# Kernel optimization log

Hardware: AMD Instinct MI355X
Metric: run time of the kernel (lower is better)

The kernel has to match this reference:

```python
import jax, jax.numpy as jnp
import numpy as np

N, D, H = 32768, 512, 8
HD = D // H  # head_dim = 64
LN_EPS = 1e-5


def setup_inputs() -> dict:
    key = jax.random.key(0)
    ks = jax.random.split(key, 5)
    s = 1.0 / np.sqrt(D)
    return {
        "h": jax.random.normal(ks[0], (N, D), dtype=jnp.float32),
        "Wq": jax.random.normal(ks[1], (D, D), dtype=jnp.float32) * s,
        "Wk": jax.random.normal(ks[2], (D, D), dtype=jnp.float32) * s,
        "Wv": jax.random.normal(ks[3], (D, D), dtype=jnp.float32) * s,
        "Wf": jax.random.normal(ks[4], (D, D), dtype=jnp.float32) * s,
        "ln_gamma": jnp.ones((D,), dtype=jnp.float32),
        "ln_beta": jnp.zeros((D,), dtype=jnp.float32),
    }


def _layernorm(x, g, b):
    mu = jnp.mean(x, axis=-1, keepdims=True)
    var = jnp.mean(jnp.square(x - mu), axis=-1, keepdims=True)
    return (x - mu) * jax.lax.rsqrt(var + LN_EPS) * g + b


def reference(h, Wq, Wk, Wv, Wf, ln_gamma, ln_beta):
    n = h.shape[0]
    # projections (torch Linear y = x @ W^T; weights here stored as [in,out])
    q = jax.nn.relu((h @ Wq).reshape(n, H, HD))
    k = jax.nn.relu((h @ Wk).reshape(n, H, HD))
    v = (h @ Wv).reshape(n, H, HD)
    # per-node outer-product accumulation over heads (n = head axis here)
    kv = jnp.einsum('bnd,bne->bde', k, v)          # [N, HD, HD]
    num = jnp.einsum('bnd,bde->bne', q, kv)        # [N, H, HD]
    denom = jnp.einsum('bnd,bd->bn', q, k.sum(axis=1))  # [N, H]
    attn = num / denom[..., None]                  # [N, H, HD]
    fh = attn.reshape(n, D) @ Wf                   # dropout = identity (eval)
    out = _layernorm(h + fh, ln_gamma, ln_beta)
    return (out, q, k, v)
```

## Files before the change

kernel.cpp:

```cpp
#include <hip/hip_runtime.h>
#include <hip/hip_bf16.h>

#define NROWS 32768
#define DIM   512
#define HEADS 8
#define LN_EPS 1e-5f

typedef __attribute__((ext_vector_type(8))) short short8;
typedef __attribute__((ext_vector_type(4))) float floatx4;

typedef __attribute__((address_space(3))) void lds_void;
typedef __attribute__((address_space(1))) void gbl_void;

__device__ __forceinline__ void async16(const void* g, void* l) {
    __builtin_amdgcn_global_load_lds(
        (gbl_void*)(unsigned long long)(uintptr_t)g,
        (lds_void*)(unsigned int)(uintptr_t)l,
        16, 0, 0);
}

__global__ __launch_bounds__(256) void hconv_kernel(
    const float* __restrict__ h, __hip_bfloat16* __restrict__ hb)
{
    const size_t i = ((size_t)blockIdx.x * 256 + threadIdx.x) * 4;
    const float4 f = *(const float4*)(h + i);
    union { ushort4 u; __hip_bfloat16 b[4]; } pk;
    pk.b[0] = __float2bfloat16(f.x);
    pk.b[1] = __float2bfloat16(f.y);
    pk.b[2] = __float2bfloat16(f.z);
    pk.b[3] = __float2bfloat16(f.w);
    *(ushort4*)(hb + i) = pk.u;
}

__global__ __launch_bounds__(256) void wtrans_kernel(
    const float* __restrict__ W, __hip_bfloat16* __restrict__ Wt)
{
    __shared__ float tile[32][33];
    const int bn = blockIdx.x * 32;
    const int bk = blockIdx.y * 32;
    const int tx = threadIdx.x & 31;
    const int ty = threadIdx.x >> 5;
    #pragma unroll
    for (int i = ty; i < 32; i += 8)
        tile[i][tx] = W[(size_t)(bk + i) * DIM + bn + tx];
    __syncthreads();
    #pragma unroll
    for (int i = ty; i < 32; i += 8)
        Wt[(size_t)(bn + i) * DIM + bk + tx] = __float2bfloat16(tile[tx][i]);
}

__global__ __launch_bounds__(256) void mfma_gemm_kernel(
    const __hip_bfloat16* __restrict__ A,
    const __hip_bfloat16* __restrict__ Bt,
    float* __restrict__ C, int relu)
{
    __shared__ __align__(16) char smem[16384];

    const int t    = threadIdx.x;
    const int lane = t & 63;
    const int w    = t >> 6;
    const int wm   = w >> 1, wn = w & 1;
    const int l16  = lane & 15, quad = lane >> 4;
    const int bm   = blockIdx.y * 128;
    const int bn   = blockIdx.x * 128;

    const int c0 = w * 128 + lane;
    const int c1 = c0 + 64;
    const int r0 = c0 >> 2, kq0 = (c0 & 3) ^ ((r0 >> 1) & 3);
    const int r1 = c1 >> 2, kq1 = (c1 & 3) ^ ((r1 >> 1) & 3);

    const __hip_bfloat16* gA0 = A  + (size_t)(bm + r0) * DIM + kq0 * 8;
    const __hip_bfloat16* gA1 = A  + (size_t)(bm + r1) * DIM + kq1 * 8;
    const __hip_bfloat16* gB0 = Bt + (size_t)(bn + r0) * DIM + kq0 * 8;
    const __hip_bfloat16* gB1 = Bt + (size_t)(bn + r1) * DIM + kq1 * 8;

    char* dA0 = smem + (w * 128 +  0) * 16;
    char* dA1 = smem + (w * 128 + 64) * 16;
    char* dB0 = smem + 8192 + (w * 128 +  0) * 16;
    char* dB1 = smem + 8192 + (w * 128 + 64) * 16;

    int aoff[4], boff[4];
    #pragma unroll
    for (int i = 0; i < 4; ++i) {
        const int ra = wm * 64 + i * 16 + l16;
        aoff[i] = (ra * 4 + (quad ^ ((ra >> 1) & 3))) * 16;
        const int rb = wn * 64 + i * 16 + l16;
        boff[i] = 8192 + (rb * 4 + (quad ^ ((rb >> 1) & 3))) * 16;
    }

    floatx4 acc[4][4];
    #pragma unroll
    for (int i = 0; i < 4; ++i)
        #pragma unroll
        for (int j = 0; j < 4; ++j)
            acc[i][j] = (floatx4){0.f, 0.f, 0.f, 0.f};

    for (int k0 = 0; k0 < DIM; k0 += 32) {
        async16(gA0 + k0, dA0);
        async16(gA1 + k0, dA1);
        async16(gB0 + k0, dB0);
        async16(gB1 + k0, dB1);
        __syncthreads();

        short8 af[4], bf[4];
        #pragma unroll
        for (int i = 0; i < 4; ++i) af[i] = *(const short8*)(smem + aoff[i]);
        #pragma unroll
        for (int j = 0; j < 4; ++j) bf[j] = *(const short8*)(smem + boff[j]);

        #pragma unroll
        for (int i = 0; i < 4; ++i)
            #pragma unroll
            for (int j = 0; j < 4; ++j)
                acc[i][j] = __builtin_amdgcn_mfma_f32_16x16x32_bf16(
                    af[i], bf[j], acc[i][j], 0, 0, 0);

        __syncthreads();
    }

    #pragma unroll
    for (int i = 0; i < 4; ++i) {
        const int gr = bm + wm * 64 + i * 16 + quad * 4;
        #pragma unroll
        for (int j = 0; j < 4; ++j) {
            const int gc = bn + wn * 64 + j * 16 + l16;
            #pragma unroll
            for (int rg = 0; rg < 4; ++rg) {
                float vv = acc[i][j][rg];
                if (relu) vv = fmaxf(vv, 0.f);
                C[(size_t)(gr + rg) * DIM + gc] = vv;
            }
        }
    }
}

__global__ __launch_bounds__(256) void attn_kernel(
    const float* __restrict__ q, const float* __restrict__ k,
    const float* __restrict__ v, __hip_bfloat16* __restrict__ attn)
{
    __shared__ float sq[2][DIM], sk[2][DIM], sv[2][DIM];
    __shared__ float skv[2][64][68];
    __shared__ float sksum[2][64];

    const int t = threadIdx.x;
    const int r = t >> 7;
    const int u = t & 127;
    const size_t base = ((size_t)blockIdx.x * 2 + r) * DIM;

    ((float4*)sq[r])[u] = ((const float4*)(q + base))[u];
    ((float4*)sk[r])[u] = ((const float4*)(k + base))[u];
    ((float4*)sv[r])[u] = ((const float4*)(v + base))[u];
    __syncthreads();

    const int e0 = (u & 15) * 4;
    const int d0 = (u >> 4) * 8;

    if (u < 64) {
        float s = 0.f;
        #pragma unroll
        for (int h = 0; h < HEADS; ++h) s += sk[r][h * 64 + u];
        sksum[r][u] = s;
    }

    float4 acc[8];
    #pragma unroll
    for (int i = 0; i < 8; ++i) acc[i] = make_float4(0.f, 0.f, 0.f, 0.f);
    #pragma unroll
    for (int h = 0; h < HEADS; ++h) {
        const float4 v4 = *(const float4*)&sv[r][h * 64 + e0];
        #pragma unroll
        for (int i = 0; i < 8; ++i) {
            const float kd = sk[r][h * 64 + d0 + i];
            acc[i].x += kd * v4.x; acc[i].y += kd * v4.y;
            acc[i].z += kd * v4.z; acc[i].w += kd * v4.w;
        }
    }
    #pragma unroll
    for (int i = 0; i < 8; ++i)
        *(float4*)&skv[r][d0 + i][e0] = acc[i];
    __syncthreads();

    const int n = u >> 4;
    float sx = 0.f, sy = 0.f, sz = 0.f, sw = 0.f, den = 0.f;
    #pragma unroll 8
    for (int d = 0; d < 64; ++d) {
        const float qd = sq[r][n * 64 + d];
        const float4 kv4 = *(const float4*)&skv[r][d][e0];
        sx += qd * kv4.x; sy += qd * kv4.y;
        sz += qd * kv4.z; sw += qd * kv4.w;
        den += qd * sksum[r][d];
    }
    union { ushort4 us; __hip_bfloat16 b[4]; } pk;
    pk.b[0] = __float2bfloat16(sx / den);
    pk.b[1] = __float2bfloat16(sy / den);
    pk.b[2] = __float2bfloat16(sz / den);
    pk.b[3] = __float2bfloat16(sw / den);
    *(ushort4*)(attn + base + n * 64 + e0) = pk.us;
}

__global__ __launch_bounds__(256) void ln_kernel(
    const float* __restrict__ h, const float* fh,
    const float* __restrict__ gamma, const float* __restrict__ beta,
    float* out)
{
    const int lane = threadIdx.x & 63;
    const int wave = threadIdx.x >> 6;
    const size_t base = ((size_t)blockIdx.x * 4 + wave) * DIM;

    float x[8];
    float s = 0.f;
    #pragma unroll
    for (int i = 0; i < 8; ++i) {
        const int j = lane + i * 64;
        x[i] = h[base + j] + fh[base + j];
        s += x[i];
    }
    #pragma unroll
    for (int off = 32; off > 0; off >>= 1) s += __shfl_down(s, off);
    const float mu = __shfl(s, 0) * (1.f / DIM);

    float vs = 0.f;
    #pragma unroll
    for (int i = 0; i < 8; ++i) { const float d = x[i] - mu; vs += d * d; }
    #pragma unroll
    for (int off = 32; off > 0; off >>= 1) vs += __shfl_down(vs, off);
    const float rstd = rsqrtf(__shfl(vs, 0) * (1.f / DIM) + LN_EPS);

    #pragma unroll
    for (int i = 0; i < 8; ++i) {
        const int j = lane + i * 64;
        out[base + j] = (x[i] - mu) * rstd * gamma[j] + beta[j];
    }
}

extern "C" void kernel_launch(void* const* d_in, const int* in_sizes, int n_in,
                              void* d_out, int out_size, void* d_ws, size_t ws_size,
                              hipStream_t stream)
{
    const float* h     = (const float*)d_in[0];
    const float* Wq    = (const float*)d_in[1];
    const float* Wk    = (const float*)d_in[2];
    const float* Wv    = (const float*)d_in[3];
    const float* Wf    = (const float*)d_in[4];
    const float* gamma = (const float*)d_in[5];
    const float* beta  = (const float*)d_in[6];

    const size_t ND = (size_t)NROWS * DIM;
    float* out = (float*)d_out;
    float* qo  = out + ND;
    float* ko  = out + 2 * ND;
    float* vo  = out + 3 * ND;
    float* fh  = out;

    __hip_bfloat16* hb  = (__hip_bfloat16*)d_ws;
    __hip_bfloat16* wtq = hb + ND;
    __hip_bfloat16* wtk = wtq + DIM * DIM;
    __hip_bfloat16* wtv = wtk + DIM * DIM;
    __hip_bfloat16* wtf = wtv + DIM * DIM;
    __hip_bfloat16* attnb = hb;

    const dim3 ggrid(DIM / 128, NROWS / 128);
    const dim3 wgrid(16, 16);

    hconv_kernel<<<NROWS * DIM / 1024, 256, 0, stream>>>(h, hb);
    wtrans_kernel<<<wgrid, 256, 0, stream>>>(Wq, wtq);
    wtrans_kernel<<<wgrid, 256, 0, stream>>>(Wk, wtk);
    wtrans_kernel<<<wgrid, 256, 0, stream>>>(Wv, wtv);
    wtrans_kernel<<<wgrid, 256, 0, stream>>>(Wf, wtf);

    mfma_gemm_kernel<<<ggrid, 256, 0, stream>>>(hb, wtq, qo, 1);
    mfma_gemm_kernel<<<ggrid, 256, 0, stream>>>(hb, wtk, ko, 1);
    mfma_gemm_kernel<<<ggrid, 256, 0, stream>>>(hb, wtv, vo, 0);

    attn_kernel<<<NROWS / 2, 256, 0, stream>>>(qo, ko, vo, attnb);

    mfma_gemm_kernel<<<ggrid, 256, 0, stream>>>(attnb, wtf, fh, 0);

    ln_kernel<<<NROWS / 4, 256, 0, stream>>>(h, fh, gamma, beta, out);
}
```

Baseline: 542.6 us.

## Reassociate attention via head scores, fuse QKV GEMM, widen K tile

Rewrites the per-node attention to compute an 8x8 q·k score matrix and weight v by normalized scores, avoiding the 64x64 kv outer-product accumulation. Merges the Q/K/V projections into one GEMM launch writing to three outputs, doubles the GEMM K-step to 64 with a wider LDS swizzle, and combines the four weight transposes into one launch. Layernorm loads/stores are vectorised to float4. Reassociation changes rounding order slightly; doubled LDS use may reduce occupancy.

```diff
diff --git a/kernel.cpp b/kernel.cpp
--- a/kernel.cpp
+++ b/kernel.cpp
@@ -33,9 +33,15 @@
 }
 
 __global__ __launch_bounds__(256) void wtrans_kernel(
-    const float* __restrict__ W, __hip_bfloat16* __restrict__ Wt)
+    const float* __restrict__ Wq, const float* __restrict__ Wk,
+    const float* __restrict__ Wv, const float* __restrict__ Wf,
+    __hip_bfloat16* __restrict__ Wt)
 {
     __shared__ float tile[32][33];
+    const int z = blockIdx.z;
+    const float* W = (z == 0) ? Wq : (z == 1) ? Wk : (z == 2) ? Wv : Wf;
+    __hip_bfloat16* dst = Wt + (size_t)z * DIM * DIM;
+
     const int bn = blockIdx.x * 32;
     const int bk = blockIdx.y * 32;
     const int tx = threadIdx.x & 31;
@@ -46,15 +52,15 @@
     __syncthreads();
     #pragma unroll
     for (int i = ty; i < 32; i += 8)
-        Wt[(size_t)(bn + i) * DIM + bk + tx] = __float2bfloat16(tile[tx][i]);
+        dst[(size_t)(bn + i) * DIM + bk + tx] = __float2bfloat16(tile[tx][i]);
 }
 
 __global__ __launch_bounds__(256) void mfma_gemm_kernel(
     const __hip_bfloat16* __restrict__ A,
     const __hip_bfloat16* __restrict__ Bt,
-    float* __restrict__ C, int relu)
-{
-    __shared__ __align__(16) char smem[16384];
+    float* __restrict__ C, int qkv)
+{
+    __shared__ __align__(16) char smem[32768];
 
     const int t    = threadIdx.x;
     const int lane = t & 63;
@@ -62,31 +68,42 @@
     const int wm   = w >> 1, wn = w & 1;
     const int l16  = lane & 15, quad = lane >> 4;
     const int bm   = blockIdx.y * 128;
-    const int bn   = blockIdx.x * 128;
-
-    const int c0 = w * 128 + lane;
-    const int c1 = c0 + 64;
-    const int r0 = c0 >> 2, kq0 = (c0 & 3) ^ ((r0 >> 1) & 3);
-    const int r1 = c1 >> 2, kq1 = (c1 & 3) ^ ((r1 >> 1) & 3);
-
-    const __hip_bfloat16* gA0 = A  + (size_t)(bm + r0) * DIM + kq0 * 8;
-    const __hip_bfloat16* gA1 = A  + (size_t)(bm + r1) * DIM + kq1 * 8;
-    const __hip_bfloat16* gB0 = Bt + (size_t)(bn + r0) * DIM + kq0 * 8;
-    const __hip_bfloat16* gB1 = Bt + (size_t)(bn + r1) * DIM + kq1 * 8;
-
-    char* dA0 = smem + (w * 128 +  0) * 16;
-    char* dA1 = smem + (w * 128 + 64) * 16;
-    char* dB0 = smem + 8192 + (w * 128 +  0) * 16;
-    char* dB1 = smem + 8192 + (w * 128 + 64) * 16;
-
-    int aoff[4], boff[4];
-    #pragma unroll
-    for (int i = 0; i < 4; ++i) {
-        const int ra = wm * 64 + i * 16 + l16;
-        aoff[i] = (ra * 4 + (quad ^ ((ra >> 1) & 3))) * 16;
-        const int rb = wn * 64 + i * 16 + l16;
-        boff[i] = 8192 + (rb * 4 + (quad ^ ((rb >> 1) & 3))) * 16;
-    }
+    const int bx   = blockIdx.x;
+    const int bn   = bx * 128;
+
+    float* Cp;
+    int ccol, relu;
+    if (qkv) {
+        Cp   = C + (size_t)(bx >> 2) * ((size_t)NROWS * DIM);
+        ccol = (bx & 3) * 128;
+        relu = (bx >> 2) < 2;
+    } else {
+        Cp = C; ccol = bn; relu = 0;
+    }
+
+    int offA[4], offB[4];
+    char* dA[4]; char* dB[4];
+    #pragma unroll
+    for (int s = 0; s < 4; ++s) {
+        const int p = w * 256 + s * 64 + lane;
+        const int r = p >> 3;
+        const int c = (p & 7) ^ (r & 7);
+        offA[s] = (bm + r) * DIM + c * 8;
+        offB[s] = (bn + r) * DIM + c * 8;
+        dA[s] = smem + (w * 256 + s * 64) * 16;
+        dB[s] = smem + 16384 + (w * 256 + s * 64) * 16;
+    }
+
+    int aoff[2][4], boff[2][4];
+    #pragma unroll
+    for (int kk = 0; kk < 2; ++kk)
+        #pragma unroll
+        for (int i = 0; i < 4; ++i) {
+            const int ra = wm * 64 + i * 16 + l16;
+            aoff[kk][i] = (ra * 8 + ((kk * 4 + quad) ^ (ra & 7))) * 16;
+            const int rb = wn * 64 + i * 16 + l16;
+            boff[kk][i] = 16384 + (rb * 8 + ((kk * 4 + quad) ^ (rb & 7))) * 16;
+        }
 
     floatx4 acc[4][4];
     #pragma unroll
@@ -95,25 +112,27 @@
         for (int j = 0; j < 4; ++j)
             acc[i][j] = (floatx4){0.f, 0.f, 0.f, 0.f};
 
-    for (int k0 = 0; k0 < DIM; k0 += 32) {
-        async16(gA0 + k0, dA0);
-        async16(gA1 + k0, dA1);
-        async16(gB0 + k0, dB0);
-        async16(gB1 + k0, dB1);
+    for (int k0 = 0; k0 < DIM; k0 += 64) {
+        #pragma unroll
+        for (int s = 0; s < 4; ++s) async16(A + offA[s] + k0, dA[s]);
+        #pragma unroll
+        for (int s = 0; s < 4; ++s) async16(Bt + offB[s] + k0, dB[s]);
         __syncthreads();
 
-        short8 af[4], bf[4];
-        #pragma unroll
-        for (int i = 0; i < 4; ++i) af[i] = *(const short8*)(smem + aoff[i]);
-        #pragma unroll
-        for (int j = 0; j < 4; ++j) bf[j] = *(const short8*)(smem + boff[j]);
-
-        #pragma unroll
-        for (int i = 0; i < 4; ++i)
+        #pragma unroll
+        for (int kk = 0; kk < 2; ++kk) {
+            short8 af[4], bf[4];
             #pragma unroll
-            for (int j = 0; j < 4; ++j)
-                acc[i][j] = __builtin_amdgcn_mfma_f32_16x16x32_bf16(
-                    af[i], bf[j], acc[i][j], 0, 0, 0);
+            for (int i = 0; i < 4; ++i) af[i] = *(const short8*)(smem + aoff[kk][i]);
+            #pragma unroll
+            for (int j = 0; j < 4; ++j) bf[j] = *(const short8*)(smem + boff[kk][j]);
+            #pragma unroll
+            for (int i = 0; i < 4; ++i)
+                #pragma unroll
+                for (int j = 0; j < 4; ++j)
+                    acc[i][j] = __builtin_amdgcn_mfma_f32_16x16x32_bf16(
+                        af[i], bf[j], acc[i][j], 0, 0, 0);
+        }
 
         __syncthreads();
     }
@@ -123,12 +142,12 @@
         const int gr = bm + wm * 64 + i * 16 + quad * 4;
         #pragma unroll
         for (int j = 0; j < 4; ++j) {
-            const int gc = bn + wn * 64 + j * 16 + l16;
+            const int gc = ccol + wn * 64 + j * 16 + l16;
             #pragma unroll
             for (int rg = 0; rg < 4; ++rg) {
                 float vv = acc[i][j][rg];
                 if (relu) vv = fmaxf(vv, 0.f);
-                C[(size_t)(gr + rg) * DIM + gc] = vv;
+                Cp[(size_t)(gr + rg) * DIM + gc] = vv;
             }
         }
     }
@@ -138,64 +157,66 @@
     const float* __restrict__ q, const float* __restrict__ k,
     const float* __restrict__ v, __hip_bfloat16* __restrict__ attn)
 {
-    __shared__ float sq[2][DIM], sk[2][DIM], sv[2][DIM];
-    __shared__ float skv[2][64][68];
-    __shared__ float sksum[2][64];
+    __shared__ float sq[4][8][68];
+    __shared__ float sk[4][8][68];
+    __shared__ float sv[4][8][68];
 
     const int t = threadIdx.x;
-    const int r = t >> 7;
-    const int u = t & 127;
-    const size_t base = ((size_t)blockIdx.x * 2 + r) * DIM;
-
-    ((float4*)sq[r])[u] = ((const float4*)(q + base))[u];
-    ((float4*)sk[r])[u] = ((const float4*)(k + base))[u];
-    ((float4*)sv[r])[u] = ((const float4*)(v + base))[u];
+    const int w = t >> 6, lane = t & 63;
+    const size_t base = ((size_t)blockIdx.x * 4 + w) * DIM;
+
+    const int sh = lane >> 3;
+    const int sd = (lane & 7) * 8;
+    {
+        const float4 q0 = ((const float4*)(q + base))[lane * 2];
+        const float4 q1 = ((const float4*)(q + base))[lane * 2 + 1];
+        const float4 k0 = ((const float4*)(k + base))[lane * 2];
+        const float4 k1 = ((const float4*)(k + base))[lane * 2 + 1];
+        const float4 v0 = ((const float4*)(v + base))[lane * 2];
+        const float4 v1 = ((const float4*)(v + base))[lane * 2 + 1];
+        *(float4*)&sq[w][sh][sd]     = q0;
+        *(float4*)&sq[w][sh][sd + 4] = q1;
+        *(float4*)&sk[w][sh][sd]     = k0;
+        *(float4*)&sk[w][sh][sd + 4] = k1;
+        *(float4*)&sv[w][sh][sd]     = v0;
+        *(float4*)&sv[w][sh][sd + 4] = v1;
+    }
     __syncthreads();
 
-    const int e0 = (u & 15) * 4;
-    const int d0 = (u >> 4) * 8;
-
-    if (u < 64) {
-        float s = 0.f;
-        #pragma unroll
-        for (int h = 0; h < HEADS; ++h) s += sk[r][h * 64 + u];
-        sksum[r][u] = s;
-    }
-
-    float4 acc[8];
-    #pragma unroll
-    for (int i = 0; i < 8; ++i) acc[i] = make_float4(0.f, 0.f, 0.f, 0.f);
-    #pragma unroll
-    for (int h = 0; h < HEADS; ++h) {
-        const float4 v4 = *(const float4*)&sv[r][h * 64 + e0];
-        #pragma unroll
-        for (int i = 0; i < 8; ++i) {
-            const float kd = sk[r][h * 64 + d0 + i];
-            acc[i].x += kd * v4.x; acc[i].y += kd * v4.y;
-            acc[i].z += kd * v4.z; acc[i].w += kd * v4.w;
-        }
-    }
-    #pragma unroll
-    for (int i = 0; i < 8; ++i)
-        *(float4*)&skv[r][d0 + i][e0] = acc[i];
-    __syncthreads();
-
-    const int n = u >> 4;
-    float sx = 0.f, sy = 0.f, sz = 0.f, sw = 0.f, den = 0.f;
-    #pragma unroll 8
-    for (int d = 0; d < 64; ++d) {
-        const float qd = sq[r][n * 64 + d];
-        const float4 kv4 = *(const float4*)&skv[r][d][e0];
-        sx += qd * kv4.x; sy += qd * kv4.y;
-        sz += qd * kv4.z; sw += qd * kv4.w;
-        den += qd * sksum[r][d];
-    }
-    union { ushort4 us; __hip_bfloat16 b[4]; } pk;
-    pk.b[0] = __float2bfloat16(sx / den);
-    pk.b[1] = __float2bfloat16(sy / den);
-    pk.b[2] = __float2bfloat16(sz / den);
-    pk.b[3] = __float2bfloat16(sw / den);
-    *(ushort4*)(attn + base + n * 64 + e0) = pk.us;
+    const int n  = lane >> 3;
+    const int hh = lane & 7;
+    float s = 0.f;
+    #pragma unroll
+    for (int d = 0; d < 64; d += 4) {
+        const float4 a = *(const float4*)&sq[w][n][d];
+        const float4 b = *(const float4*)&sk[w][hh][d];
+        s += a.x * b.x + a.y * b.y + a.z * b.z + a.w * b.w;
+    }
+    float den = s;
+    den += __shfl_xor(den, 1);
+    den += __shfl_xor(den, 2);
+    den += __shfl_xor(den, 4);
+    const float p = s / den;
+
+    float pl[8];
+    #pragma unroll
+    for (int h = 0; h < 8; ++h) pl[h] = __shfl(p, (lane & 56) | h);
+
+    const int eg = (lane & 7) * 8;
+    float o[8] = {0.f, 0.f, 0.f, 0.f, 0.f, 0.f, 0.f, 0.f};
+    #pragma unroll
+    for (int h = 0; h < 8; ++h) {
+        const float4 v0 = *(const float4*)&sv[w][h][eg];
+        const float4 v1 = *(const float4*)&sv[w][h][eg + 4];
+        o[0] += pl[h] * v0.x; o[1] += pl[h] * v0.y;
+        o[2] += pl[h] * v0.z; o[3] += pl[h] * v0.w;
+        o[4] += pl[h] * v1.x; o[5] += pl[h] * v1.y;
+        o[6] += pl[h] * v1.z; o[7] += pl[h] * v1.w;
+    }
+    union { short8 s8; __hip_bfloat16 b[8]; } pk;
+    #pragma unroll
+    for (int j = 0; j < 8; ++j) pk.b[j] = __float2bfloat16(o[j]);
+    *(short8*)(attn + base + (size_t)lane * 8) = pk.s8;
 }
 
 __global__ __launch_bounds__(256) void ln_kernel(
@@ -207,14 +228,18 @@
     const int wave = threadIdx.x >> 6;
     const size_t base = ((size_t)blockIdx.x * 4 + wave) * DIM;
 
+    const float4 a0 = ((const float4*)(h + base))[lane * 2];
+    const float4 a1 = ((const float4*)(h + base))[lane * 2 + 1];
+    const float4 b0 = ((const float4*)(fh + base))[lane * 2];
+    const float4 b1 = ((const float4*)(fh + base))[lane * 2 + 1];
+
     float x[8];
+    x[0] = a0.x + b0.x; x[1] = a0.y + b0.y; x[2] = a0.z + b0.z; x[3] = a0.w + b0.w;
+    x[4] = a1.x + b1.x; x[5] = a1.y + b1.y; x[6] = a1.z + b1.z; x[7] = a1.w + b1.w;
+
     float s = 0.f;
     #pragma unroll
-    for (int i = 0; i < 8; ++i) {
-        const int j = lane + i * 64;
-        x[i] = h[base + j] + fh[base + j];
-        s += x[i];
-    }
+    for (int i = 0; i < 8; ++i) s += x[i];
     #pragma unroll
     for (int off = 32; off > 0; off >>= 1) s += __shfl_down(s, off);
     const float mu = __shfl(s, 0) * (1.f / DIM);
@@ -226,11 +251,23 @@
     for (int off = 32; off > 0; off >>= 1) vs += __shfl_down(vs, off);
     const float rstd = rsqrtf(__shfl(vs, 0) * (1.f / DIM) + LN_EPS);
 
-    #pragma unroll
-    for (int i = 0; i < 8; ++i) {
-        const int j = lane + i * 64;
-        out[base + j] = (x[i] - mu) * rstd * gamma[j] + beta[j];
-    }
+    const float4 g0 = ((const float4*)gamma)[lane * 2];
+    const float4 g1 = ((const float4*)gamma)[lane * 2 + 1];
+    const float4 e0 = ((const float4*)beta)[lane * 2];
+    const float4 e1 = ((const float4*)beta)[lane * 2 + 1];
+
+    float4 r0, r1;
+    r0.x = (x[0] - mu) * rstd * g0.x + e0.x;
+    r0.y = (x[1] - mu) * rstd * g0.y + e0.y;
+    r0.z = (x[2] - mu) * rstd * g0.z + e0.z;
+    r0.w = (x[3] - mu) * rstd * g0.w + e0.w;
+    r1.x = (x[4] - mu) * rstd * g1.x + e1.x;
+    r1.y = (x[5] - mu) * rstd * g1.y + e1.y;
+    r1.z = (x[6] - mu) * rstd * g1.z + e1.z;
+    r1.w = (x[7] - mu) * rstd * g1.w + e1.w;
+
+    ((float4*)(out + base))[lane * 2]     = r0;
+    ((float4*)(out + base))[lane * 2 + 1] = r1;
 }
 
 extern "C" void kernel_launch(void* const* d_in, const int* in_sizes, int n_in,
@@ -253,28 +290,18 @@
     float* fh  = out;
 
     __hip_bfloat16* hb  = (__hip_bfloat16*)d_ws;
-    __hip_bfloat16* wtq = hb + ND;
-    __hip_bfloat16* wtk = wtq + DIM * DIM;
-    __hip_bfloat16* wtv = wtk + DIM * DIM;
-    __hip_bfloat16* wtf = wtv + DIM * DIM;
+    __hip_bfloat16* wt  = hb + ND;
+    __hip_bfloat16* wtf = wt + 3 * DIM * DIM;
     __hip_bfloat16* attnb = hb;
 
-    const dim3 ggrid(DIM / 128, NROWS / 128);
-    const dim3 wgrid(16, 16);
-
     hconv_kernel<<<NROWS * DIM / 1024, 256, 0, stream>>>(h, hb);
-    wtrans_kernel<<<wgrid, 256, 0, stream>>>(Wq, wtq);
-    wtrans_kernel<<<wgrid, 256, 0, stream>>>(Wk, wtk);
-    wtrans_kernel<<<wgrid, 256, 0, stream>>>(Wv, wtv);
-    wtrans_kernel<<<wgrid, 256, 0, stream>>>(Wf, wtf);
-
-    mfma_gemm_kernel<<<ggrid, 256, 0, stream>>>(hb, wtq, qo, 1);
-    mfma_gemm_kernel<<<ggrid, 256, 0, stream>>>(hb, wtk, ko, 1);
-    mfma_gemm_kernel<<<ggrid, 256, 0, stream>>>(hb, wtv, vo, 0);
-
-    attn_kernel<<<NROWS / 2, 256, 0, stream>>>(qo, ko, vo, attnb);
-
-    mfma_gemm_kernel<<<ggrid, 256, 0, stream>>>(attnb, wtf, fh, 0);
+    wtrans_kernel<<<dim3(16, 16, 4), 256, 0, stream>>>(Wq, Wk, Wv, Wf, wt);
+
+    mfma_gemm_kernel<<<dim3(12, NROWS / 128), 256, 0, stream>>>(hb, wt, qo, 1);
+
+    attn_kernel<<<NROWS / 4, 256, 0, stream>>>(qo, ko, vo, attnb);
+
+    mfma_gemm_kernel<<<dim3(4, NROWS / 128), 256, 0, stream>>>(attnb, wtf, fh, 0);
 
     ln_kernel<<<NROWS / 4, 256, 0, stream>>>(h, fh, gamma, beta, out);
 }
```

Result: faster. 465.5 us (-14.2%).
